# Kernel tuning notes

Hardware: AMD Instinct MI355X
Metric: run time of the kernel (lower is better)

The kernel has to match this reference:

```python
import jax, jax.numpy as jnp
import numpy as np

ANGRES = 5  # u = v = angRes, n = 25


def _l2norm(x, axis):
    n = jnp.sqrt(jnp.sum(x * x, axis=axis, keepdims=True))
    return x / jnp.maximum(n, 1e-12)  # matches torch F.normalize eps


def _cos_attn(qm, km, vm):
    # qm: (b, M, K), km: (b, K, M), vm: (b, M, K)
    q = _l2norm(qm, -1)
    k = _l2norm(km, -2)
    att = jax.nn.softmax(q @ k, axis=-1)  # (b, M, M)
    return att @ vm


def _af_attn(x, u, v):  # AngularFrequencyAttention: b c (u v) h w -> b (c u) (h v w)
    b, c, n, h, w = x.shape
    t = x.reshape(b, c, u, v, h, w)
    qm = t.transpose(0, 1, 2, 4, 3, 5).reshape(b, c * u, h * v * w)   # (b,c,u,h,v,w)
    km = t.transpose(0, 4, 3, 5, 1, 2).reshape(b, h * v * w, c * u)   # (b,h,v,w,c,u)
    o = _cos_attn(qm, km, qm)
    o = o.reshape(b, c, u, h, v, w).transpose(0, 1, 2, 4, 3, 5).reshape(b, c, n, h, w)
    return o + x


def _sa_attn(x, u, v):  # SpatialAngularAttention: b c (u v) h w -> b (h u) (c v w)
    b, c, n, h, w = x.shape
    t = x.reshape(b, c, u, v, h, w)
    qm = t.transpose(0, 4, 2, 1, 3, 5).reshape(b, h * u, c * v * w)   # (b,h,u,c,v,w)
    km = t.transpose(0, 1, 3, 5, 4, 2).reshape(b, c * v * w, h * u)   # (b,c,v,w,h,u)
    o = _cos_attn(qm, km, qm)
    o = o.reshape(b, h, u, c, v, w).transpose(0, 3, 2, 4, 1, 5).reshape(b, c, n, h, w)
    return o + x


def _sf_attn(x, u, v):  # SpatialFrequencyAttention: b c (u v) h w -> b (c h) (w u v)
    b, c, n, h, w = x.shape
    t = x.reshape(b, c, u, v, h, w)
    qm = t.transpose(0, 1, 4, 5, 2, 3).reshape(b, c * h, w * u * v)   # (b,c,h,w,u,v)
    km = t.transpose(0, 5, 2, 3, 1, 4).reshape(b, w * u * v, c * h)   # (b,w,u,v,c,h)
    o = _cos_attn(qm, km, qm)
    o = o.reshape(b, c, h, w, u, v).transpose(0, 1, 4, 5, 2, 3).reshape(b, c, n, h, w)
    return o + x


def _layernorm(x, g, bta, eps=1e-5):
    mu = jnp.mean(x, -1, keepdims=True)
    var = jnp.mean(jnp.square(x - mu), -1, keepdims=True)
    return (x - mu) * jax.lax.rsqrt(var + eps) * g + bta


def setup_inputs() -> dict:
    key = jax.random.key(0)
    k0, k1, k2 = jax.random.split(key, 3)
    b, c, n, h, w = 4, 64, 25, 48, 48
    x = jax.random.normal(k0, (b, c, n, h, w), dtype=jnp.float32)
    gamma = jnp.ones((3 * c,), dtype=jnp.float32)
    beta = jnp.zeros((3 * c,), dtype=jnp.float32)
    w1 = jax.random.normal(k1, (3 * c, c), dtype=jnp.float32) * 0.02
    w2 = jax.random.normal(k2, (c, c), dtype=jnp.float32) * 0.02
    return {"x": x, "gamma": gamma, "beta": beta, "w1": w1, "w2": w2}


def reference(x, gamma, beta, w1, w2):
    u = v = ANGRES
    b, c, n, h, w = x.shape
    sf = _sf_attn(x, u, v)
    af = _af_attn(x, u, v)
    sa = _sa_attn(x, u, v)
    cat = jnp.concatenate([sf, af, sa], axis=1)            # (b, 3c, n, h, w)
    f = cat.transpose(0, 3, 4, 2, 1).reshape(b * h * w, n, 3 * c)
    y = _layernorm(f, gamma, beta)
    y = jax.nn.relu(y @ w1) @ w2                            # (bhw, n, c); dropout p=0.01 is eval-identity
    out = y.reshape(b, h, w, n, c).transpose(0, 4, 3, 1, 2) + x
    return out
```

## Files before the change

kernel.cpp:

```cpp
#include <hip/hip_runtime.h>
#include <stdint.h>

typedef __attribute__((ext_vector_type(8))) short bf16x8;
typedef __attribute__((ext_vector_type(4))) float f32x4;

__device__ __forceinline__ float b2f(short s) {
  union { unsigned u; float f; } a; a.u = ((unsigned)(unsigned short)s) << 16; return a.f;
}
__device__ __forceinline__ short f2b(float f) {
  union { float f; unsigned u; } a; a.f = f;
  unsigned r = a.u + 0x7fffu + ((a.u >> 16) & 1u);
  return (short)(r >> 16);
}
__device__ __forceinline__ void gload16(const void* g, void* l) {
  __builtin_amdgcn_global_load_lds((__attribute__((address_space(1))) void*)g,
                                   (__attribute__((address_space(3))) void*)l, 16, 0, 0);
}

#define SWZ(row, col) ((col) ^ (((row) & 7) << 3))

__global__ __launch_bounds__(256) void permute_sf_k(const float* __restrict__ x,
                                                    short* __restrict__ Q,
                                                    float* __restrict__ inv) {
  __shared__ float buf[4][1200];
  int wave = threadIdx.x >> 6, lane = threadIdx.x & 63;
  int gr = blockIdx.x * 4 + wave;
  int b = gr / 3072, m = gr - b * 3072;
  int c = m / 48, hh = m - c * 48;
  const float* xb = x + (long)(b * 64 + c) * 57600 + hh * 48;
  for (int uv = 0; uv < 25; ++uv)
    if (lane < 48) buf[wave][uv * 48 + lane] = xb[uv * 2304 + lane];
  __syncthreads();
  short* Qr = Q + (long)gr * 1280;
  float ss = 0.f;
  for (int k = lane; k < 1280; k += 64) {
    float v = 0.f;
    if (k < 1200) { int wv = k / 25, uv = k - wv * 25; v = buf[wave][uv * 48 + wv]; }
    ss += v * v;
    Qr[k] = f2b(v);
  }
  #pragma unroll
  for (int o = 32; o >= 1; o >>= 1) ss += __shfl_xor(ss, o, 64);
  if (lane == 0) inv[gr] = 1.0f / fmaxf(sqrtf(ss), 1e-12f);
}

__global__ __launch_bounds__(256) void transpose_k(const short* __restrict__ in, short* __restrict__ out,
                                                   int R, int C) {
  __shared__ short t[32][33];
  long base = (long)blockIdx.z * R * C;
  int c0 = blockIdx.x * 32, r0 = blockIdx.y * 32;
  int tx = threadIdx.x & 31, ty = threadIdx.x >> 5;
  #pragma unroll
  for (int i = 0; i < 32; i += 8)
    t[ty + i][tx] = in[base + (long)(r0 + ty + i) * C + c0 + tx];
  __syncthreads();
  #pragma unroll
  for (int i = 0; i < 32; i += 8)
    out[base + (long)(c0 + ty + i) * R + r0 + tx] = t[tx][ty + i];
}

__global__ __launch_bounds__(256) void permtr_all_k(const float* __restrict__ x,
    short* __restrict__ Qaf, short* __restrict__ QTaf,
    short* __restrict__ Qsa, short* __restrict__ QTsa,
    float* __restrict__ ssaf, float* __restrict__ sssa) {
  __shared__ short t[32][33];
  int bid = blockIdx.x;
  int isAF = (bid < 17280);
  int M, Mp, Kp, kt, mt, b;
  short *Q, *QT; float* ss;
  if (isAF) { M = 320; Mp = 384; Kp = 11520; kt = bid % 360; int r = bid / 360; mt = r % 12; b = r / 12;
              Q = Qaf; QT = QTaf; ss = ssaf; }
  else { int id = bid - 17280; M = 240; Mp = 256; Kp = 15360; kt = id % 480; int r = id / 480; mt = r % 8; b = r / 8;
         Q = Qsa; QT = QTsa; ss = sssa; }
  int k0 = kt * 32, m0 = mt * 32;
  int tx = threadIdx.x & 31, ty = threadIdx.x >> 5;
  const float* xb = x + (long)b * 3686400;
  #pragma unroll
  for (int i = 0; i < 32; i += 8) {
    int m = m0 + ty + i, k = k0 + tx;
    float v = 0.f;
    if (m < M) {
      int q1 = k / 240, r2 = k - q1 * 240;
      int v5 = r2 / 48, wv = r2 - v5 * 48;
      int a1 = m / 5, u = m - a1 * 5;
      long xi = isAF ? ((long)a1 * 25 + u * 5 + v5) * 2304 + q1 * 48 + wv
                     : ((long)q1 * 25 + u * 5 + v5) * 2304 + a1 * 48 + wv;
      v = xb[xi];
    }
    t[ty + i][tx] = f2b(v);
  }
  __syncthreads();
  long Qb = (long)b * Mp * Kp;
  #pragma unroll
  for (int i = 0; i < 32; i += 8)
    Q[Qb + (long)(m0 + ty + i) * Kp + k0 + tx] = t[ty + i][tx];
  #pragma unroll
  for (int i = 0; i < 32; i += 8)
    QT[Qb + (long)(k0 + ty + i) * Mp + m0 + tx] = t[tx][ty + i];
  if (threadIdx.x < 32 && m0 + (int)threadIdx.x < M) {
    float s = 0.f;
    #pragma unroll
    for (int k = 0; k < 32; ++k) { float f = b2f(t[threadIdx.x][k]); s += f * f; }
    atomicAdd(&ss[b * Mp + m0 + threadIdx.x], s);
  }
}

__global__ __launch_bounds__(256, 2) void gemm1_tri_k(const short* __restrict__ Q,
                                                      const float* __restrict__ invn,
                                                      short* __restrict__ att,
                                                      float* __restrict__ rowsum) {
  __shared__ short sm[32768];
  int tid = threadIdx.x, wave = tid >> 6, lane = tid & 63;
  int la = lane & 15, lb = lane >> 4;
  int bat = blockIdx.z;
  int bx;
  { int xcd = blockIdx.x & 7, j = blockIdx.x >> 3;
    bx = (xcd < 4) ? xcd * 38 + j : 152 + (xcd - 4) * 37 + j; }
  int yt = 0, rem = bx;
  while (rem >= 24 - yt) { rem -= 24 - yt; ++yt; }
  int xt = yt + rem;
  const short* Qb = Q + (long)bat * 3932160L;
  const float* inv = invn + (long)bat * 3072;
  int row0 = yt * 128, col0 = xt * 128;
  f32x4 acc[4][4] = {};
  int wr = wave >> 1, wc = wave & 1;
  int rloc = tid >> 3, cbase = (tid & 7) * 8;
  int ldsoff = tid * 8;

  const short *pA[4], *pB[4];
  #pragma unroll
  for (int p = 0; p < 4; ++p) {
    int row = p * 32 + rloc;
    int sc = SWZ(row, cbase);
    pA[p] = Qb + (long)(row0 + row) * 1280 + sc;
    pB[p] = Qb + (long)(col0 + row) * 1280 + sc;
  }

  #define TRI_STAGE(KT, BUF) { \
    short* Asb = sm + (BUF) * 16384; \
    short* Bsb = Asb + 8192; \
    _Pragma("unroll") \
    for (int p = 0; p < 4; ++p) { \
      gload16(pA[p] + (KT) * 64, (void*)(Asb + p * 2048 + ldsoff)); \
      gload16(pB[p] + (KT) * 64, (void*)(Bsb + p * 2048 + ldsoff)); \
    } }
  #define TRI_COMP(BUF) { \
    const short* Asb = sm + (BUF) * 16384; \
    const short* Bsb = Asb + 8192; \
    _Pragma("unroll") \
    for (int kk = 0; kk < 64; kk += 32) { \
      bf16x8 av[4], bv[4]; \
      _Pragma("unroll") \
      for (int m = 0; m < 4; ++m) \
        av[m] = *(const bf16x8*)&Asb[(wr * 64 + m * 16 + la) * 64 + SWZ(la, kk + lb * 8)]; \
      _Pragma("unroll") \
      for (int nn = 0; nn < 4; ++nn) \
        bv[nn] = *(const bf16x8*)&Bsb[(wc * 64 + nn * 16 + la) * 64 + SWZ(la, kk + lb * 8)]; \
      _Pragma("unroll") \
      for (int m = 0; m < 4; ++m) \
        _Pragma("unroll") \
        for (int nn = 0; nn < 4; ++nn) \
          acc[m][nn] = __builtin_amdgcn_mfma_f32_16x16x32_bf16(av[m], bv[nn], acc[m][nn], 0, 0, 0); \
    } }

  TRI_STAGE(0, 0)
  for (int kt = 0; kt < 19; ++kt) {
    TRI_STAGE(kt + 1, (kt + 1) & 1)
    asm volatile("s_waitcnt vmcnt(8)" ::: "memory");
    __builtin_amdgcn_s_barrier();
    TRI_COMP(kt & 1)
    asm volatile("" ::: "memory");
    __builtin_amdgcn_s_barrier();
  }
  asm volatile("s_waitcnt vmcnt(0)" ::: "memory");
  __builtin_amdgcn_s_barrier();
  TRI_COMP(1)
  asm volatile("" ::: "memory");
  __builtin_amdgcn_s_barrier();

  short* staged = sm;
  #pragma unroll
  for (int m = 0; m < 4; ++m) {
    #pragma unroll
    for (int nn = 0; nn < 4; ++nn) {
      int cl = wc * 64 + nn * 16 + la;
      float ic = inv[col0 + cl];
      #pragma unroll
      for (int j = 0; j < 4; ++j) {
        int rl = wr * 64 + m * 16 + lb * 4 + j;
        staged[rl * 136 + cl] = f2b(__expf(acc[m][nn][j] * inv[row0 + rl] * ic));
      }
    }
  }
  __syncthreads();
  short* attb = att + (long)bat * 9437184L;
  float* rsb = rowsum + (long)bat * 3072;
  {
    int r = tid >> 1, half = tid & 1;
    short* dst = attb + (long)(row0 + r) * 3072 + col0 + half * 64;
    const short* src = &staged[r * 136 + half * 64];
    float s = 0.f;
    #pragma unroll
    for (int q = 0; q < 8; ++q) {
      bf16x8 v = *(const bf16x8*)&src[q * 8];
      *(bf16x8*)&dst[q * 8] = v;
      #pragma unroll
      for (int jj = 0; jj < 8; ++jj) s += b2f(v[jj]);
    }
    s += __shfl_xor(s, 1, 64);
    if (half == 0) atomicAdd(&rsb[row0 + r], s);
  }
  if (xt != yt) {
    int c = tid >> 1, half = tid & 1;
    short* dst = attb + (long)(col0 + c) * 3072 + row0 + half * 64;
    float s = 0.f;
    #pragma unroll
    for (int q = 0; q < 8; ++q) {
      bf16x8 o;
      #pragma unroll
      for (int jj = 0; jj < 8; ++jj) {
        o[jj] = staged[(half * 64 + q * 8 + jj) * 136 + c];
        s += b2f(o[jj]);
      }
      *(bf16x8*)&dst[q * 8] = o;
    }
    s += __shfl_xor(s, 1, 64);
    if (half == 0) atomicAdd(&rsb[col0 + c], s);
  }
}

__global__ __launch_bounds__(256, 2) void gemm_s_all_k(
    const short* __restrict__ Aaf, const short* __restrict__ Asa,
    float* __restrict__ Sfaf, float* __restrict__ Sfsa)
{
  __shared__ short sm[32768];
  int bid = blockIdx.x;
  const short* A; float* Sf;
  int lda, ktotal, ksper, ldc, row0, col0, bat, kc;
  long sA, sS;
  if (bid < 288) {
    int txy = bid % 9, z = bid / 9;
    col0 = (txy % 3) * 128; row0 = (txy / 3) * 128;
    bat = z / 8; kc = z % 8;
    lda = 11520; ktotal = 180; ksper = 23; ldc = 384;
    sA = 4423680L; sS = 147456L; A = Aaf; Sf = Sfaf;
  } else {
    int id = bid - 288;
    int txy = id % 4, z = id / 4;
    col0 = (txy % 2) * 128; row0 = (txy / 2) * 128;
    bat = z / 16; kc = z % 16;
    lda = 15360; ktotal = 240; ksper = 15; ldc = 256;
    sA = 3932160L; sS = 65536L; A = Asa; Sf = Sfsa;
  }
  int tid = threadIdx.x;
  int wave = tid >> 6, lane = tid & 63;
  int la = lane & 15, lb = lane >> 4;
  const short* Ab = A + (long)bat * sA;
  int kb = kc * ksper, ke = min(ktotal, kb + ksper);
  int L = ke - kb;
  f32x4 acc[4][4] = {};
  int wr = wave >> 1, wc = wave & 1;
  int rloc = tid >> 3, cbase = (tid & 7) * 8;
  int ldsoff = tid * 8;

  const short *pA[4], *pB[4];
  #pragma unroll
  for (int p = 0; p < 4; ++p) {
    int row = p * 32 + rloc;
    int sc = SWZ(row, cbase);
    pA[p] = Ab + (long)(row0 + row) * lda + sc;
    pB[p] = Ab + (long)(col0 + row) * lda + sc;
  }

  #define GS_STAGE(KT, BUF) { \
    short* Asb = sm + (BUF) * 16384; \
    short* Bsb = Asb + 8192; \
    _Pragma("unroll") \
    for (int p = 0; p < 4; ++p) { \
      gload16(pA[p] + (KT) * 64, (void*)(Asb + p * 2048 + ldsoff)); \
      gload16(pB[p] + (KT) * 64, (void*)(Bsb + p * 2048 + ldsoff)); \
    } }
  #define GS_COMP(BUF) { \
    const short* Asb = sm + (BUF) * 16384; \
    const short* Bsb = Asb + 8192; \
    _Pragma("unroll") \
    for (int kk = 0; kk < 64; kk += 32) { \
      bf16x8 av[4], bv[4]; \
      _Pragma("unroll") \
      for (int m = 0; m < 4; ++m) \
        av[m] = *(const bf16x8*)&Asb[(wr * 64 + m * 16 + la) * 64 + SWZ(la, kk + lb * 8)]; \
      _Pragma("unroll") \
      for (int nn = 0; nn < 4; ++nn) \
        bv[nn] = *(const bf16x8*)&Bsb[(wc * 64 + nn * 16 + la) * 64 + SWZ(la, kk + lb * 8)]; \
      _Pragma("unroll") \
      for (int m = 0; m < 4; ++m) \
        _Pragma("unroll") \
        for (int nn = 0; nn < 4; ++nn) \
          acc[m][nn] = __builtin_amdgcn_mfma_f32_16x16x32_bf16(av[m], bv[nn], acc[m][nn], 0, 0, 0); \
    } }

  GS_STAGE(kb, 0)
  for (int t = 0; t < L - 1; ++t) {
    GS_STAGE(kb + t + 1, (t + 1) & 1)
    asm volatile("s_waitcnt vmcnt(8)" ::: "memory");
    __builtin_amdgcn_s_barrier();
    GS_COMP(t & 1)
    asm volatile("" ::: "memory");
    __builtin_amdgcn_s_barrier();
  }
  asm volatile("s_waitcnt vmcnt(0)" ::: "memory");
  __builtin_amdgcn_s_barrier();
  GS_COMP((L - 1) & 1)

  float* Sb = Sf + (long)bat * sS;
  #pragma unroll
  for (int m = 0; m < 4; ++m) {
    int gr0 = row0 + wr * 64 + m * 16 + lb * 4;
    #pragma unroll
    for (int nn = 0; nn < 4; ++nn) {
      int gc = col0 + wc * 64 + nn * 16 + la;
      #pragma unroll
      for (int j = 0; j < 4; ++j)
        atomicAdd(&Sb[(long)(gr0 + j) * ldc + gc], acc[m][nn][j]);
    }
  }
}

__global__ __launch_bounds__(256) void softmax_all_k(
    const float* __restrict__ Sfaf, const float* __restrict__ Sfsa,
    const float* __restrict__ ssaf, const float* __restrict__ sssa,
    short* __restrict__ attaf, short* __restrict__ attsa)
{
  int wave = threadIdx.x >> 6, lane = threadIdx.x & 63;
  int rid = blockIdx.x * 4 + wave;
  int row, b, Mv, Mp; const float *Sf, *ss; short* att;
  if (rid < 1280) { row = rid % 320; b = rid / 320; Mv = 320; Mp = 384; Sf = Sfaf; ss = ssaf; att = attaf; }
  else { int id = rid - 1280; row = id % 240; b = id / 240; Mv = 240; Mp = 256; Sf = Sfsa; ss = sssa; att = attsa; }
  long sS = (long)Mp * Mp;
  const float* Sr = Sf + (long)b * sS + (long)row * Mp;
  const float* ssb = ss + b * Mp;
  float inv_i = rsqrtf(fmaxf(ssb[row], 1e-24f));
  float ev[6] = {0.f, 0.f, 0.f, 0.f, 0.f, 0.f};
  float sum = 0.f;
  #pragma unroll
  for (int q = 0; q < 6; ++q) {
    int j = q * 64 + lane;
    if (j < Mv) {
      float e = __expf(Sr[j] * inv_i * rsqrtf(fmaxf(ssb[j], 1e-24f)));
      ev[q] = e; sum += e;
    }
  }
  #pragma unroll
  for (int o = 32; o >= 1; o >>= 1) sum += __shfl_xor(sum, o, 64);
  float rden = 1.0f / sum;
  short* ar = att + (long)b * sS + (long)row * Mp;
  #pragma unroll
  for (int q = 0; q < 6; ++q) {
    int j = q * 64 + lane;
    if (j < Mp) ar[j] = (j < Mv) ? f2b(ev[q] * rden) : (short)0;
  }
}

__global__ __launch_bounds__(512) void gemm2sf_k(const short* __restrict__ A,
                                                 const short* __restrict__ B,
                                                 const float* __restrict__ rowsum,
                                                 short* __restrict__ F) {
  __shared__ short sm[65536];
  int tid = threadIdx.x;
  int wave = tid >> 6, lane = tid & 63;
  int la = lane & 15, lb = lane >> 4;
  int wr = wave >> 2, wc = wave & 3;
  int wk;
  { int xcd = blockIdx.x & 7, j = blockIdx.x >> 3; wk = xcd * 30 + j; }
  int yt = wk % 12, rem = wk / 12;
  int xt = rem % 5, bat = rem / 5;
  const short* Ab = A + (long)bat * 9437184L;
  const short* Bb = B + (long)bat * 3932160L;
  int rloc = tid >> 3;
  int cbase = (tid & 7) * 8;
  int sc = cbase ^ ((rloc & 7) << 3);
  const short *pAg[4], *pBg[4];
  #pragma unroll
  for (int g = 0; g < 4; ++g) {
    pAg[g] = Ab + (long)(rloc * 48 + yt * 4 + g) * 3072 + sc;
    pBg[g] = Bb + (long)(xt * 256 + g * 64 + rloc) * 3072 + sc;
  }
  f32x4 acc[8][4] = {};

  #pragma unroll
  for (int g = 0; g < 4; ++g) {
    gload16(pAg[g], (void*)(sm + g * 4096 + tid * 8));
    gload16(pBg[g], (void*)(sm + 16384 + g * 4096 + tid * 8));
  }
  asm volatile("s_waitcnt vmcnt(0)" ::: "memory");
  __builtin_amdgcn_s_barrier();

  #define G2_PHASE(MH, KK, LOADB) { \
    if (LOADB) { \
      _Pragma("unroll") \
      for (int nn = 0; nn < 4; ++nn) \
        bv[nn] = *(const bf16x8*)&Bsb[(wc * 64 + nn * 16 + la) * 64 + SWZ(la, (KK) + lb * 8)]; \
    } \
    _Pragma("unroll") \
    for (int m = 0; m < 4; ++m) \
      av[m] = *(const bf16x8*)&Asb[(wr * 128 + (MH) * 64 + m * 16 + la) * 64 + SWZ(la, (KK) + lb * 8)]; \
    __builtin_amdgcn_s_setprio(1); \
    _Pragma("unroll") \
    for (int m = 0; m < 4; ++m) \
      _Pragma("unroll") \
      for (int nn = 0; nn < 4; ++nn) \
        acc[(MH) * 4 + m][nn] = __builtin_amdgcn_mfma_f32_16x16x32_bf16(av[m], bv[nn], acc[(MH) * 4 + m][nn], 0, 0, 0); \
    __builtin_amdgcn_s_setprio(0); \
  }

  for (int t = 0; t < 48; ++t) {
    const short* Asb = sm + (t & 1) * 32768;
    const short* Bsb = Asb + 16384;
    short* An = sm + ((t + 1) & 1) * 32768;
    short* Bn = An + 16384;
    int k1 = (t + 1) * 64;
    bool pf = (t < 47);
    bf16x8 av[4], bv[4];

    asm volatile("s_waitcnt vmcnt(2)" ::: "memory");
    __builtin_amdgcn_s_barrier();
    if (pf) { gload16(pBg[0] + k1, (void*)(Bn + tid * 8));
              gload16(pBg[1] + k1, (void*)(Bn + 4096 + tid * 8)); }
    G2_PHASE(0, 0, 1)
    if (pf) asm volatile("s_waitcnt vmcnt(2)" ::: "memory");
    else    asm volatile("s_waitcnt vmcnt(0)" ::: "memory");
    __builtin_amdgcn_s_barrier();
    if (pf) { gload16(pBg[2] + k1, (void*)(Bn + 8192 + tid * 8));
              gload16(pBg[3] + k1, (void*)(Bn + 12288 + tid * 8)); }
    G2_PHASE(1, 0, 0)
    asm volatile("s_waitcnt vmcnt(4)" ::: "memory");
    __builtin_amdgcn_s_barrier();
    if (pf) { gload16(pAg[0] + k1, (void*)(An + tid * 8));
              gload16(pAg[2] + k1, (void*)(An + 8192 + tid * 8)); }
    G2_PHASE(0, 32, 1)
    asm volatile("s_waitcnt vmcnt(6)" ::: "memory");
    __builtin_amdgcn_s_barrier();
    if (pf) { gload16(pAg[1] + k1, (void*)(An + 4096 + tid * 8));
              gload16(pAg[3] + k1, (void*)(An + 12288 + tid * 8)); }
    G2_PHASE(1, 32, 0)
  }
  __syncthreads();

  const float* rsb = rowsum + (long)bat * 3072;
  float rs[8][4];
  #pragma unroll
  for (int m = 0; m < 8; ++m) {
    int sub = wr * 2 + (m >> 2);
    #pragma unroll
    for (int j = 0; j < 4; ++j) {
      int cc = (m & 3) * 16 + lb * 4 + j;
      rs[m][j] = 1.0f / rsb[cc * 48 + yt * 4 + sub];
    }
  }
  short* staged = sm;
  #pragma unroll
  for (int m = 0; m < 8; ++m) {
    int sub = wr * 2 + (m >> 2);
    #pragma unroll
    for (int nn = 0; nn < 4; ++nn) {
      int gcl = wc * 64 + nn * 16 + la;
      int chunk = gcl * 4 + sub;
      int key = (gcl & 7) << 3;
      short4 o;
      o.x = f2b(acc[m][nn][0] * rs[m][0]); o.y = f2b(acc[m][nn][1] * rs[m][1]);
      o.z = f2b(acc[m][nn][2] * rs[m][2]); o.w = f2b(acc[m][nn][3] * rs[m][3]);
      *(short4*)&staged[chunk * 64 + (((m & 3) * 16 + lb * 4) ^ key)] = o;
    }
  }
  __syncthreads();
  #pragma unroll
  for (int i = 0; i < 16; ++i) {
    int chunk = i * 64 + (tid >> 3);
    int part = tid & 7;
    int gcl = chunk >> 2, sub = chunk & 3;
    int key = (gcl & 7) << 3;
    bf16x8 v = *(const bf16x8*)&staged[chunk * 64 + ((part * 8) ^ key)];
    int gc = xt * 256 + gcl;
    if (gc < 1200) {
      int hh = yt * 4 + sub;
      int wv = gc / 25, nidx = gc - wv * 25;
      long base = (((long)(bat * 48 + hh) * 48 + wv) * 25 + nidx) * 192 + part * 8;
      *(bf16x8*)&F[base] = v;
    }
  }
}

__global__ __launch_bounds__(256) void gemm2_afsa_k(
    const short* __restrict__ attaf, const short* __restrict__ QTaf,
    const short* __restrict__ attsa, const short* __restrict__ QTsa,
    short* __restrict__ F)
{
  __shared__ short sm[20480];
  short* As = sm;
  short* Bs = sm + 4096;
  int bid = blockIdx.x;
  int isAF = (bid < 900);
  int NX, NY, LDA, KST, wk;
  const short *A, *B; long SA, SB;
  if (isAF) {
    NX = 45; NY = 5; LDA = 384; KST = 6; SA = 147456L; SB = 4423680L; A = attaf; B = QTaf;
    int xcd = bid & 7, j = bid >> 3;
    wk = (xcd < 4) ? xcd * 113 + j : 4 * 113 + (xcd - 4) * 112 + j;
  } else {
    NX = 60; NY = 4; LDA = 256; KST = 4; SA = 65536L; SB = 3932160L; A = attsa; B = QTsa;
    int id = bid - 900;
    int xcd = id & 7, j = id >> 3;
    wk = xcd * 120 + j;
  }
  int yt = wk % NY, rem = wk / NY;
  int xt = rem % NX, bat = rem / NX;
  int tid = threadIdx.x, wave = tid >> 6, lane = tid & 63;
  int la = lane & 15, lb = lane >> 4;
  const short* Ab = A + (long)bat * SA;
  const short* Bb = B + (long)bat * SB;
  f32x4 acc[4][4] = {};
  int rloc = tid >> 3, cbase = (tid & 7) * 8;
  int ldsoff = tid * 8;

  const short *pA[2], *pB[8];
  #pragma unroll
  for (int p = 0; p < 2; ++p) {
    int r = p * 32 + rloc;
    int sc = SWZ(r, cbase);
    int rowg = isAF ? (r * 5 + yt) : (yt * 64 + r);
    pA[p] = Ab + (long)rowg * LDA + sc;
  }
  #pragma unroll
  for (int p = 0; p < 8; ++p) {
    int rb = p * 32 + rloc;
    int sc = SWZ(rb, cbase);
    int rowg;
    if (isAF) rowg = xt * 256 + rb;
    else { int c = rb & 63, g = rb >> 6; rowg = c * 240 + xt * 4 + g; }
    pB[p] = Bb + (long)rowg * LDA + sc;
  }

  for (int kt = 0; kt < KST; ++kt) {
    #pragma unroll
    for (int p = 0; p < 2; ++p)
      gload16(pA[p] + kt * 64, (void*)(As + p * 2048 + ldsoff));
    #pragma unroll
    for (int p = 0; p < 8; ++p)
      gload16(pB[p] + kt * 64, (void*)(Bs + p * 2048 + ldsoff));
    __syncthreads();
    #pragma unroll
    for (int kk = 0; kk < 64; kk += 32) {
      bf16x8 av[4], bv[4];
      #pragma unroll
      for (int m = 0; m < 4; ++m)
        av[m] = *(const bf16x8*)&As[(m * 16 + la) * 64 + SWZ(la, kk + lb * 8)];
      #pragma unroll
      for (int nn = 0; nn < 4; ++nn)
        bv[nn] = *(const bf16x8*)&Bs[(wave * 64 + nn * 16 + la) * 64 + SWZ(la, kk + lb * 8)];
      #pragma unroll
      for (int m = 0; m < 4; ++m)
        #pragma unroll
        for (int nn = 0; nn < 4; ++nn)
          acc[m][nn] = __builtin_amdgcn_mfma_f32_16x16x32_bf16(av[m], bv[nn], acc[m][nn], 0, 0, 0);
    }
    __syncthreads();
  }

  short* staged = sm;
  #pragma unroll
  for (int m = 0; m < 4; ++m) {
    #pragma unroll
    for (int nn = 0; nn < 4; ++nn) {
      if (!isAF) {
        #pragma unroll
        for (int j = 0; j < 4; ++j)
          staged[((m * 16 + lb * 4 + j) * 4 + wave) * 72 + nn * 16 + la] = f2b(acc[m][nn][j]);
      } else {
        short4 o;
        o.x = f2b(acc[m][nn][0]); o.y = f2b(acc[m][nn][1]);
        o.z = f2b(acc[m][nn][2]); o.w = f2b(acc[m][nn][3]);
        *(short4*)&staged[(wave * 64 + nn * 16 + la) * 72 + m * 16 + lb * 4] = o;
      }
    }
  }
  __syncthreads();

  #pragma unroll
  for (int rd = 0; rd < 8; ++rd) {
    int chunk = rd * 32 + (tid >> 3);
    int part = tid & 7;
    bf16x8 v = *(const bf16x8*)&staged[chunk * 72 + part * 8];
    long base; bool ok = true;
    if (isAF) {
      int gc = xt * 256 + chunk;
      int hh = gc / 240, r2 = gc - hh * 240, v5 = r2 / 48, wv = r2 - v5 * 48;
      base = (((long)(bat * 48 + hh) * 48 + wv) * 25 + yt * 5 + v5) * 192 + 64 + part * 8;
    } else {
      int r = chunk >> 2, g = chunk & 3;
      int gr = yt * 64 + r; ok = (gr < 240);
      int hh = gr / 5, u = gr - hh * 5;
      int r2 = xt * 4 + g, v5 = r2 / 48, wv = r2 - v5 * 48;
      base = (((long)(bat * 48 + hh) * 48 + wv) * 25 + u * 5 + v5) * 192 + 128 + part * 8;
    }
    if (ok) *(bf16x8*)&F[base] = v;
  }
}

__global__ __launch_bounds__(256) void prep_w_k(const float* __restrict__ w1, const float* __restrict__ w2,
                                                short* __restrict__ w1t, short* __restrict__ w2t) {
  int idx = blockIdx.x * 256 + threadIdx.x;
  if (idx < 12288) {
    int i = idx / 64, j = idx - i * 64;
    w1t[j * 192 + i] = f2b(w1[idx]);
  } else if (idx < 16384) {
    int k = idx - 12288;
    int i = k / 64, j = k - i * 64;
    w2t[j * 64 + i] = f2b(w2[k]);
  }
}

__global__ __launch_bounds__(256) void ln_mlp_mfma_k(
    const short* __restrict__ F, const float* __restrict__ x,
    const float* __restrict__ gamma, const float* __restrict__ beta,
    const short* __restrict__ w1t, const short* __restrict__ w2t,
    float* __restrict__ out)
{
  int n = blockIdx.x, hh = blockIdx.y, b = blockIdx.z;
  __shared__ short A1[48 * 200];
  __shared__ float xs[64 * 49];
  __shared__ __align__(16) char pool[19584];
  short* Fs = (short*)pool;
  short* Y1 = (short*)pool;
  float* Y2 = (float*)(pool + 6912);
  int tid = threadIdx.x, wave = tid >> 6, lane = tid & 63;
  int la = lane & 15, lb = lane >> 4;
  long Fb0 = ((long)(b * 48 + hh) * 1200 + n) * 192;
  long xb = (long)b * 3686400 + (long)n * 2304 + hh * 48;

  #pragma unroll
  for (int it = 0; it < 5; ++it) {
    int ci = tid + 256 * it;
    if (ci < 1152) {
      int r = ci / 24, q = ci - r * 24;
      gload16(&F[Fb0 + (long)r * 4800 + q * 8], (void*)(Fs + ci * 8));
    }
  }
  {
    int ch = tid >> 2, qq = tid & 3;
    const float* xr = x + xb + (long)ch * 57600 + qq * 12;
    #pragma unroll
    for (int i = 0; i < 12; ++i) xs[ch * 49 + qq * 12 + i] = xr[i];
  }
  __syncthreads();

  float g0 = gamma[lane], g1 = gamma[lane + 64], g2 = gamma[lane + 128];
  float bt0 = beta[lane], bt1 = beta[lane + 64], bt2 = beta[lane + 128];
  #pragma unroll 4
  for (int rr = 0; rr < 12; ++rr) {
    int r = wave * 12 + rr;
    float xv = xs[lane * 49 + r];
    float v0 = b2f(Fs[r * 192 + lane]) + xv;
    float v1 = b2f(Fs[r * 192 + lane + 64]) + xv;
    float v2 = b2f(Fs[r * 192 + lane + 128]) + xv;
    float s = v0 + v1 + v2;
    #pragma unroll
    for (int o = 32; o >= 1; o >>= 1) s += __shfl_xor(s, o, 64);
    float mu = s * (1.f / 192.f);
    float d0 = v0 - mu, d1 = v1 - mu, d2 = v2 - mu;
    float q = d0 * d0 + d1 * d1 + d2 * d2;
    #pragma unroll
    for (int o = 32; o >= 1; o >>= 1) q += __shfl_xor(q, o, 64);
    float rsq = rsqrtf(q * (1.f / 192.f) + 1e-5f);
    A1[r * 200 + lane]       = f2b(d0 * rsq * g0 + bt0);
    A1[r * 200 + lane + 64]  = f2b(d1 * rsq * g1 + bt1);
    A1[r * 200 + lane + 128] = f2b(d2 * rsq * g2 + bt2);
  }
  __syncthreads();

  f32x4 acc1[3] = {};
  #pragma unroll
  for (int ks = 0; ks < 6; ++ks) {
    bf16x8 bv = *(const bf16x8*)&w1t[(wave * 16 + la) * 192 + ks * 32 + lb * 8];
    #pragma unroll
    for (int m = 0; m < 3; ++m) {
      bf16x8 av = *(const bf16x8*)&A1[(m * 16 + la) * 200 + ks * 32 + lb * 8];
      acc1[m] = __builtin_amdgcn_mfma_f32_16x16x32_bf16(av, bv, acc1[m], 0, 0, 0);
    }
  }
  #pragma unroll
  for (int m = 0; m < 3; ++m)
    #pragma unroll
    for (int j = 0; j < 4; ++j)
      Y1[(m * 16 + lb * 4 + j) * 72 + wave * 16 + la] = f2b(fmaxf(acc1[m][j], 0.f));
  __syncthreads();

  f32x4 acc2[3] = {};
  #pragma unroll
  for (int ks = 0; ks < 2; ++ks) {
    bf16x8 bv = *(const bf16x8*)&w2t[(wave * 16 + la) * 64 + ks * 32 + lb * 8];
    #pragma unroll
    for (int m = 0; m < 3; ++m) {
      bf16x8 av = *(const bf16x8*)&Y1[(m * 16 + la) * 72 + ks * 32 + lb * 8];
      acc2[m] = __builtin_amdgcn_mfma_f32_16x16x32_bf16(av, bv, acc2[m], 0, 0, 0);
    }
  }
  #pragma unroll
  for (int m = 0; m < 3; ++m)
    #pragma unroll
    for (int j = 0; j < 4; ++j)
      Y2[(m * 16 + lb * 4 + j) * 66 + wave * 16 + la] = acc2[m][j];
  __syncthreads();

  #pragma unroll
  for (int i = 0; i < 12; ++i) {
    int e = tid + 256 * i;
    int cc = e / 48, wv = e - cc * 48;
    out[xb + (long)cc * 57600 + wv] = Y2[wv * 66 + cc] + xs[cc * 49 + wv];
  }
}

extern "C" void kernel_launch(void* const* d_in, const int* in_sizes, int n_in,
                              void* d_out, int out_size, void* d_ws, size_t ws_size,
                              hipStream_t stream) {
  (void)in_sizes; (void)n_in; (void)out_size;
  const float* x     = (const float*)d_in[0];
  const float* gamma = (const float*)d_in[1];
  const float* beta  = (const float*)d_in[2];
  const float* w1    = (const float*)d_in[3];
  const float* w2    = (const float*)d_in[4];
  float* out = (float*)d_out;

  const size_t NEED = 237191168UL;
  if (ws_size < NEED) return;
  char* ws = (char*)d_ws;
  short* F     = (short*)(ws);
  short* attsf = (short*)(ws + 88473600UL);
  short* Qsf   = (short*)(ws + 163971072UL);
  short* QTsf  = (short*)(ws + 199360512UL);
  float* rowsum = (float*)(ws + 234749952UL);
  float* invn  = (float*)(ws + 237109248UL);
  short* w1t   = (short*)(ws + 237158400UL);
  short* w2t   = (short*)(ws + 237182976UL);
  short* Qaf   = (short*)(ws + 88473600UL);
  short* QTaf  = (short*)(ws + 123863040UL);
  float* Sfsa  = (float*)(ws + 159252480UL);
  float* ssaf  = (float*)(ws + 160301056UL);
  float* sssa  = (float*)(ws + 160307200UL);
  short* attaf = (short*)(ws + 160311296UL);
  short* attsa = (short*)(ws + 161490944UL);
  short* Qsa   = (short*)(ws + 163971072UL);
  short* QTsa  = (short*)(ws + 195428352UL);
  float* Sfaf  = (float*)(ws + 234749952UL);

  prep_w_k<<<64, 256, 0, stream>>>(w1, w2, w1t, w2t);

  permute_sf_k<<<3072, 256, 0, stream>>>(x, Qsf, invn);
  transpose_k<<<dim3(40, 96, 4), 256, 0, stream>>>(Qsf, QTsf, 3072, 1280);
  hipMemsetAsync(rowsum, 0, 49152, stream);
  gemm1_tri_k<<<dim3(300, 1, 4), 256, 0, stream>>>(Qsf, invn, attsf, rowsum);
  gemm2sf_k<<<dim3(240), 512, 0, stream>>>(attsf, QTsf, rowsum, F);

  hipMemsetAsync(Sfaf, 0, 2359296, stream);
  hipMemsetAsync((char*)Sfsa, 0, 1058816, stream);
  permtr_all_k<<<32640, 256, 0, stream>>>(x, Qaf, QTaf, Qsa, QTsa, ssaf, sssa);
  gemm_s_all_k<<<544, 256, 0, stream>>>(Qaf, Qsa, Sfaf, Sfsa);
  softmax_all_k<<<560, 256, 0, stream>>>(Sfaf, Sfsa, ssaf, sssa, attaf, attsa);
  gemm2_afsa_k<<<1860, 256, 0, stream>>>(attaf, QTaf, attsa, QTsa, F);

  ln_mlp_mfma_k<<<dim3(25, 48, 4), 256, 0, stream>>>(F, x, gamma, beta, w1t, w2t, out);
}
```

Measured before the change: 465.8 us.

## Retile SF symmetric QK^T gemm to 256x256 tiles with 512 threads

The triangular Q·Q^T gemm for the SF branch moves from 128x128 tiles on 256 threads to 256x256 tiles on 512 threads. It reuses the phased prefetch pipeline from the second gemm, which is now a shared macro, and maps 78 tiles per batch across XCDs. The goal is more data reuse per LDS load and fewer blocks overall. Row and column sums are now taken from register partials with shuffles instead of re-reading staged data, and the staged tile is stored transposed with a swizzle. The cost is 128KB of LDS and a larger accumulator set, which limits occupancy to one block per CU and leaves a coarser tail.

```diff
diff --git a/kernel.cpp b/kernel.cpp
--- a/kernel.cpp
+++ b/kernel.cpp
@@ -18,6 +18,24 @@
 }
 
 #define SWZ(row, col) ((col) ^ (((row) & 7) << 3))
+
+#define G2_PHASE(MH, KK, LOADB) { \
+    if (LOADB) { \
+      _Pragma("unroll") \
+      for (int nn = 0; nn < 4; ++nn) \
+        bv[nn] = *(const bf16x8*)&Bsb[(wc * 64 + nn * 16 + la) * 64 + SWZ(la, (KK) + lb * 8)]; \
+    } \
+    _Pragma("unroll") \
+    for (int m = 0; m < 4; ++m) \
+      av[m] = *(const bf16x8*)&Asb[(wr * 128 + (MH) * 64 + m * 16 + la) * 64 + SWZ(la, (KK) + lb * 8)]; \
+    __builtin_amdgcn_s_setprio(1); \
+    _Pragma("unroll") \
+    for (int m = 0; m < 4; ++m) \
+      _Pragma("unroll") \
+      for (int nn = 0; nn < 4; ++nn) \
+        acc[(MH) * 4 + m][nn] = __builtin_amdgcn_mfma_f32_16x16x32_bf16(av[m], bv[nn], acc[(MH) * 4 + m][nn], 0, 0, 0); \
+    __builtin_amdgcn_s_setprio(0); \
+  }
 
 __global__ __launch_bounds__(256) void permute_sf_k(const float* __restrict__ x,
                                                     short* __restrict__ Q,
@@ -105,127 +123,144 @@
   }
 }
 
-__global__ __launch_bounds__(256, 2) void gemm1_tri_k(const short* __restrict__ Q,
-                                                      const float* __restrict__ invn,
-                                                      short* __restrict__ att,
-                                                      float* __restrict__ rowsum) {
-  __shared__ short sm[32768];
-  int tid = threadIdx.x, wave = tid >> 6, lane = tid & 63;
+__global__ __launch_bounds__(512) void gemm1_tri_k(const short* __restrict__ Q,
+                                                   const float* __restrict__ invn,
+                                                   short* __restrict__ att,
+                                                   float* __restrict__ rowsum) {
+  __shared__ short sm[65536];
+  int tid = threadIdx.x;
+  int wave = tid >> 6, lane = tid & 63;
   int la = lane & 15, lb = lane >> 4;
-  int bat = blockIdx.z;
-  int bx;
-  { int xcd = blockIdx.x & 7, j = blockIdx.x >> 3;
-    bx = (xcd < 4) ? xcd * 38 + j : 152 + (xcd - 4) * 37 + j; }
-  int yt = 0, rem = bx;
-  while (rem >= 24 - yt) { rem -= 24 - yt; ++yt; }
+  int wr = wave >> 2, wc = wave & 3;
+  int wk;
+  { int xcd = blockIdx.x & 7, j = blockIdx.x >> 3; wk = xcd * 39 + j; }
+  int bat = wk / 78, t78 = wk - bat * 78;
+  int yt = 0, rem = t78;
+  while (rem >= 12 - yt) { rem -= 12 - yt; ++yt; }
   int xt = yt + rem;
   const short* Qb = Q + (long)bat * 3932160L;
-  const float* inv = invn + (long)bat * 3072;
-  int row0 = yt * 128, col0 = xt * 128;
-  f32x4 acc[4][4] = {};
-  int wr = wave >> 1, wc = wave & 1;
-  int rloc = tid >> 3, cbase = (tid & 7) * 8;
-  int ldsoff = tid * 8;
-
-  const short *pA[4], *pB[4];
-  #pragma unroll
-  for (int p = 0; p < 4; ++p) {
-    int row = p * 32 + rloc;
-    int sc = SWZ(row, cbase);
-    pA[p] = Qb + (long)(row0 + row) * 1280 + sc;
-    pB[p] = Qb + (long)(col0 + row) * 1280 + sc;
-  }
-
-  #define TRI_STAGE(KT, BUF) { \
-    short* Asb = sm + (BUF) * 16384; \
-    short* Bsb = Asb + 8192; \
-    _Pragma("unroll") \
-    for (int p = 0; p < 4; ++p) { \
-      gload16(pA[p] + (KT) * 64, (void*)(Asb + p * 2048 + ldsoff)); \
-      gload16(pB[p] + (KT) * 64, (void*)(Bsb + p * 2048 + ldsoff)); \
-    } }
-  #define TRI_COMP(BUF) { \
-    const short* Asb = sm + (BUF) * 16384; \
-    const short* Bsb = Asb + 8192; \
-    _Pragma("unroll") \
-    for (int kk = 0; kk < 64; kk += 32) { \
-      bf16x8 av[4], bv[4]; \
-      _Pragma("unroll") \
-      for (int m = 0; m < 4; ++m) \
-        av[m] = *(const bf16x8*)&Asb[(wr * 64 + m * 16 + la) * 64 + SWZ(la, kk + lb * 8)]; \
-      _Pragma("unroll") \
-      for (int nn = 0; nn < 4; ++nn) \
-        bv[nn] = *(const bf16x8*)&Bsb[(wc * 64 + nn * 16 + la) * 64 + SWZ(la, kk + lb * 8)]; \
-      _Pragma("unroll") \
-      for (int m = 0; m < 4; ++m) \
-        _Pragma("unroll") \
-        for (int nn = 0; nn < 4; ++nn) \
-          acc[m][nn] = __builtin_amdgcn_mfma_f32_16x16x32_bf16(av[m], bv[nn], acc[m][nn], 0, 0, 0); \
-    } }
-
-  TRI_STAGE(0, 0)
-  for (int kt = 0; kt < 19; ++kt) {
-    TRI_STAGE(kt + 1, (kt + 1) & 1)
-    asm volatile("s_waitcnt vmcnt(8)" ::: "memory");
-    __builtin_amdgcn_s_barrier();
-    TRI_COMP(kt & 1)
-    asm volatile("" ::: "memory");
-    __builtin_amdgcn_s_barrier();
+  int row0 = yt * 256, col0 = xt * 256;
+  int rloc = tid >> 3;
+  int cbase = (tid & 7) * 8;
+  int sc = cbase ^ ((rloc & 7) << 3);
+  const short *pAg[4], *pBg[4];
+  #pragma unroll
+  for (int g = 0; g < 4; ++g) {
+    pAg[g] = Qb + (long)(row0 + g * 64 + rloc) * 1280 + sc;
+    pBg[g] = Qb + (long)(col0 + g * 64 + rloc) * 1280 + sc;
+  }
+  f32x4 acc[8][4] = {};
+
+  #pragma unroll
+  for (int g = 0; g < 4; ++g) {
+    gload16(pAg[g], (void*)(sm + g * 4096 + tid * 8));
+    gload16(pBg[g], (void*)(sm + 16384 + g * 4096 + tid * 8));
   }
   asm volatile("s_waitcnt vmcnt(0)" ::: "memory");
   __builtin_amdgcn_s_barrier();
-  TRI_COMP(1)
-  asm volatile("" ::: "memory");
-  __builtin_amdgcn_s_barrier();
-
+
+  for (int t = 0; t < 20; ++t) {
+    const short* Asb = sm + (t & 1) * 32768;
+    const short* Bsb = Asb + 16384;
+    short* An = sm + ((t + 1) & 1) * 32768;
+    short* Bn = An + 16384;
+    int k1 = (t + 1) * 64;
+    bool pf = (t < 19);
+    bf16x8 av[4], bv[4];
+
+    asm volatile("s_waitcnt vmcnt(2)" ::: "memory");
+    __builtin_amdgcn_s_barrier();
+    if (pf) { gload16(pBg[0] + k1, (void*)(Bn + tid * 8));
+              gload16(pBg[1] + k1, (void*)(Bn + 4096 + tid * 8)); }
+    G2_PHASE(0, 0, 1)
+    if (pf) asm volatile("s_waitcnt vmcnt(2)" ::: "memory");
+    else    asm volatile("s_waitcnt vmcnt(0)" ::: "memory");
+    __builtin_amdgcn_s_barrier();
+    if (pf) { gload16(pBg[2] + k1, (void*)(Bn + 8192 + tid * 8));
+              gload16(pBg[3] + k1, (void*)(Bn + 12288 + tid * 8)); }
+    G2_PHASE(1, 0, 0)
+    asm volatile("s_waitcnt vmcnt(4)" ::: "memory");
+    __builtin_amdgcn_s_barrier();
+    if (pf) { gload16(pAg[0] + k1, (void*)(An + tid * 8));
+              gload16(pAg[2] + k1, (void*)(An + 8192 + tid * 8)); }
+    G2_PHASE(0, 32, 1)
+    asm volatile("s_waitcnt vmcnt(6)" ::: "memory");
+    __builtin_amdgcn_s_barrier();
+    if (pf) { gload16(pAg[1] + k1, (void*)(An + 4096 + tid * 8));
+              gload16(pAg[3] + k1, (void*)(An + 12288 + tid * 8)); }
+    G2_PHASE(1, 32, 0)
+  }
+  __syncthreads();
+
+  const float* inv = invn + (long)bat * 3072;
+  float* rsb = rowsum + (long)bat * 3072;
+  short* attb = att + (long)bat * 9437184L;
+  float invc[4];
+  #pragma unroll
+  for (int nn = 0; nn < 4; ++nn) invc[nn] = inv[col0 + wc * 64 + nn * 16 + la];
   short* staged = sm;
-  #pragma unroll
-  for (int m = 0; m < 4; ++m) {
+  float cp[4] = {0.f, 0.f, 0.f, 0.f};
+  #pragma unroll
+  for (int m = 0; m < 8; ++m) {
+    int rbase = wr * 128 + (m >> 2) * 64 + (m & 3) * 16 + lb * 4;
+    float ir0 = inv[row0 + rbase], ir1 = inv[row0 + rbase + 1];
+    float ir2 = inv[row0 + rbase + 2], ir3 = inv[row0 + rbase + 3];
+    float rp0 = 0.f, rp1 = 0.f, rp2 = 0.f, rp3 = 0.f;
     #pragma unroll
     for (int nn = 0; nn < 4; ++nn) {
-      int cl = wc * 64 + nn * 16 + la;
-      float ic = inv[col0 + cl];
-      #pragma unroll
-      for (int j = 0; j < 4; ++j) {
-        int rl = wr * 64 + m * 16 + lb * 4 + j;
-        staged[rl * 136 + cl] = f2b(__expf(acc[m][nn][j] * inv[row0 + rl] * ic));
-      }
-    }
-  }
-  __syncthreads();
-  short* attb = att + (long)bat * 9437184L;
-  float* rsb = rowsum + (long)bat * 3072;
+      int c = wc * 64 + nn * 16 + la;
+      int key = (c & 7) << 3;
+      short s0 = f2b(__expf(acc[m][nn][0] * ir0 * invc[nn]));
+      short s1 = f2b(__expf(acc[m][nn][1] * ir1 * invc[nn]));
+      short s2 = f2b(__expf(acc[m][nn][2] * ir2 * invc[nn]));
+      short s3 = f2b(__expf(acc[m][nn][3] * ir3 * invc[nn]));
+      float p0 = b2f(s0), p1 = b2f(s1), p2 = b2f(s2), p3 = b2f(s3);
+      rp0 += p0; rp1 += p1; rp2 += p2; rp3 += p3;
+      cp[nn] += p0 + p1 + p2 + p3;
+      short4 o; o.x = s0; o.y = s1; o.z = s2; o.w = s3;
+      *(short4*)&staged[c * 256 + (rbase ^ key)] = o;
+    }
+    float rr[4] = {rp0, rp1, rp2, rp3};
+    #pragma unroll
+    for (int j = 0; j < 4; ++j) {
+      float s = rr[j];
+      s += __shfl_xor(s, 1, 64); s += __shfl_xor(s, 2, 64);
+      s += __shfl_xor(s, 4, 64); s += __shfl_xor(s, 8, 64);
+      if (la == 0) atomicAdd(&rsb[row0 + rbase + j], s);
+    }
+  }
+  if (xt != yt) {
+    #pragma unroll
+    for (int nn = 0; nn < 4; ++nn) {
+      float s = cp[nn];
+      s += __shfl_xor(s, 16, 64); s += __shfl_xor(s, 32, 64);
+      if (lb == 0) atomicAdd(&rsb[col0 + wc * 64 + nn * 16 + la], s);
+    }
+  }
+  __syncthreads();
+
   {
     int r = tid >> 1, half = tid & 1;
-    short* dst = attb + (long)(row0 + r) * 3072 + col0 + half * 64;
-    const short* src = &staged[r * 136 + half * 64];
-    float s = 0.f;
-    #pragma unroll
-    for (int q = 0; q < 8; ++q) {
-      bf16x8 v = *(const bf16x8*)&src[q * 8];
+    short* dst = attb + (long)(row0 + r) * 3072 + col0 + half * 128;
+    #pragma unroll
+    for (int q = 0; q < 16; ++q) {
+      bf16x8 v;
+      #pragma unroll
+      for (int jj = 0; jj < 8; ++jj) {
+        int c = half * 128 + q * 8 + jj;
+        v[jj] = staged[c * 256 + (r ^ ((c & 7) << 3))];
+      }
       *(bf16x8*)&dst[q * 8] = v;
-      #pragma unroll
-      for (int jj = 0; jj < 8; ++jj) s += b2f(v[jj]);
-    }
-    s += __shfl_xor(s, 1, 64);
-    if (half == 0) atomicAdd(&rsb[row0 + r], s);
+    }
   }
   if (xt != yt) {
     int c = tid >> 1, half = tid & 1;
-    short* dst = attb + (long)(col0 + c) * 3072 + row0 + half * 64;
-    float s = 0.f;
-    #pragma unroll
-    for (int q = 0; q < 8; ++q) {
-      bf16x8 o;
-      #pragma unroll
-      for (int jj = 0; jj < 8; ++jj) {
-        o[jj] = staged[(half * 64 + q * 8 + jj) * 136 + c];
-        s += b2f(o[jj]);
-      }
-      *(bf16x8*)&dst[q * 8] = o;
-    }
-    s += __shfl_xor(s, 1, 64);
-    if (half == 0) atomicAdd(&rsb[col0 + c], s);
+    short* dst = attb + (long)(col0 + c) * 3072 + row0 + half * 128;
+    int key = (c & 7) << 3;
+    const short* src = &staged[c * 256];
+    #pragma unroll
+    for (int q = 0; q < 16; ++q)
+      *(bf16x8*)&dst[q * 8] = *(const bf16x8*)&src[(half * 128 + q * 8) ^ key];
   }
 }
 
@@ -395,24 +430,6 @@
   asm volatile("s_waitcnt vmcnt(0)" ::: "memory");
   __builtin_amdgcn_s_barrier();
 
-  #define G2_PHASE(MH, KK, LOADB) { \
-    if (LOADB) { \
-      _Pragma("unroll") \
-      for (int nn = 0; nn < 4; ++nn) \
-        bv[nn] = *(const bf16x8*)&Bsb[(wc * 64 + nn * 16 + la) * 64 + SWZ(la, (KK) + lb * 8)]; \
-    } \
-    _Pragma("unroll") \
-    for (int m = 0; m < 4; ++m) \
-      av[m] = *(const bf16x8*)&Asb[(wr * 128 + (MH) * 64 + m * 16 + la) * 64 + SWZ(la, (KK) + lb * 8)]; \
-    __builtin_amdgcn_s_setprio(1); \
-    _Pragma("unroll") \
-    for (int m = 0; m < 4; ++m) \
-      _Pragma("unroll") \
-      for (int nn = 0; nn < 4; ++nn) \
-        acc[(MH) * 4 + m][nn] = __builtin_amdgcn_mfma_f32_16x16x32_bf16(av[m], bv[nn], acc[(MH) * 4 + m][nn], 0, 0, 0); \
-    __builtin_amdgcn_s_setprio(0); \
-  }
-
   for (int t = 0; t < 48; ++t) {
     const short* Asb = sm + (t & 1) * 32768;
     const short* Bsb = Asb + 16384;
@@ -757,7 +774,7 @@
   permute_sf_k<<<3072, 256, 0, stream>>>(x, Qsf, invn);
   transpose_k<<<dim3(40, 96, 4), 256, 0, stream>>>(Qsf, QTsf, 3072, 1280);
   hipMemsetAsync(rowsum, 0, 49152, stream);
-  gemm1_tri_k<<<dim3(300, 1, 4), 256, 0, stream>>>(Qsf, invn, attsf, rowsum);
+  gemm1_tri_k<<<dim3(312), 512, 0, stream>>>(Qsf, invn, attsf, rowsum);
   gemm2sf_k<<<dim3(240), 512, 0, stream>>>(attsf, QTsf, rowsum, F);
 
   hipMemsetAsync(Sfaf, 0, 2359296, stream);
```

Result: slower. 486.6 us (+4.5%).
